# Optimization experiments

Measured on AMD Instinct MI355X. Metric: run time of the kernel, lower is better.

Reference implementation:

```python
import jax, jax.numpy as jnp
import numpy as np

H = 56; W = 56; WS = 7; NW = WS * WS  # 49 tokens per window
HEADS = 8; DIM = 256; HIDDEN = 4 * DIM
SHIFT = NW // 2  # gilbert shift = 24 (shift_size > 0)
SCALE = (DIM // HEADS) ** -0.5
EPS = 1e-5


def _sgn(v):
    return -1 if v < 0 else 1 if v > 0 else 0


def _generate2d(x, y, ax, ay, bx, by, result):
    w = abs(ax + ay); h = abs(bx + by)
    dax, day = _sgn(ax), _sgn(ay); dbx, dby = _sgn(bx), _sgn(by)
    if h == 1 or w == 1:
        if h == 1:
            for _ in range(w):
                result.append((x, y)); x, y = x + dax, y + day
        elif w == 1:
            for _ in range(h):
                result.append((x, y)); x, y = x + dbx, y + dby
        return
    ax2, ay2 = ax // 2, ay // 2; bx2, by2 = bx // 2, by // 2
    w2 = abs(ax2 + ay2); h2 = abs(bx2 + by2)
    if 2 * w > 3 * h:
        if w2 % 2 and w > 2:
            ax2, ay2 = ax2 + dax, ay2 + day
        _generate2d(x, y, ax2, ay2, bx, by, result)
        _generate2d(x + ax2, y + ay2, ax - ax2, ay - ay2, bx, by, result)
    else:
        if h2 % 2 and h > 2:
            bx2, by2 = bx2 + dbx, by2 + dby
        _generate2d(x, y, bx2, by2, ax2, ay2, result)
        _generate2d(x + bx2, y + by2, ax, ay, bx - bx2, by - by2, result)
        _generate2d(x + (ax - dax) + (bx2 - dbx), y + (ay - day) + (by2 - dby),
                    -bx2, -by2, -(ax - ax2), -(ay - ay2), result)


def _gilbert2d(width, height):
    result = []
    if width >= height:
        _generate2d(0, 0, width, 0, 0, height, result)
    else:
        _generate2d(0, 0, 0, height, width, 0, result)
    return result


def _make_rel_index():
    # reverse_map[idx] = (y, x) for gilbert position idx
    path = _gilbert2d(W, H)
    rev = np.zeros((H * W, 2), dtype=np.int64)
    for i, (px, py) in enumerate(path[:H * W]):
        rev[i, 0] = py; rev[i, 1] = px
    pos = np.roll(rev, SHIFT, axis=0)  # shifted block: roll positions by ws^2//2
    n_windows = (H * W) // NW
    pos = pos[:n_windows * NW].reshape(n_windows, NW, 2)
    dh = pos[:, :, 0][:, :, None] - pos[:, :, 0][:, None, :] + (H - 1)
    dw = pos[:, :, 1][:, :, None] - pos[:, :, 1][:, None, :] + (W - 1)
    return (dh * (2 * W - 1) + dw).astype(np.int32)  # (nW, 49, 49)


def setup_inputs() -> dict:
    key = jax.random.key(0)
    ks = jax.random.split(key, 8)
    B, L, C = 32, H * W, DIM
    return {
        "x": jax.random.normal(ks[0], (B, L, C), jnp.float32),
        "qkv_w": jax.random.normal(ks[1], (C, 3 * C), jnp.float32) * 0.02,
        "qkv_b": jnp.zeros((3 * C,), jnp.float32),
        "proj_w": jax.random.normal(ks[2], (C, C), jnp.float32) * 0.02,
        "proj_b": jnp.zeros((C,), jnp.float32),
        "bias_table": jax.random.normal(ks[3], ((2 * H - 1) * (2 * W - 1), HEADS), jnp.float32) * 0.02,
        "norm1_w": jnp.ones((C,), jnp.float32),
        "norm1_b": jnp.zeros((C,), jnp.float32),
        "norm2_w": jnp.ones((C,), jnp.float32),
        "norm2_b": jnp.zeros((C,), jnp.float32),
        "fc1_w": jax.random.normal(ks[4], (C, HIDDEN), jnp.float32) * 0.02,
        "fc1_b": jnp.zeros((HIDDEN,), jnp.float32),
        "fc2_w": jax.random.normal(ks[5], (HIDDEN, C), jnp.float32) * 0.02,
        "fc2_b": jnp.zeros((C,), jnp.float32),
        "rel_index": jnp.asarray(_make_rel_index()),
    }


def _layernorm(x, w, b):
    mu = jnp.mean(x, axis=-1, keepdims=True)
    var = jnp.mean(jnp.square(x - mu), axis=-1, keepdims=True)
    return (x - mu) * jax.lax.rsqrt(var + EPS) * w + b


def reference(x, qkv_w, qkv_b, proj_w, proj_b, bias_table,
              norm1_w, norm1_b, norm2_w, norm2_b,
              fc1_w, fc1_b, fc2_w, fc2_b, rel_index):
    B, L, C = x.shape
    n_win = L // NW
    hd = C // HEADS

    shortcut = x
    h = _layernorm(x, norm1_w, norm1_b)
    # gilbert forward shift along the curve, then window partition
    h = jnp.roll(h, SHIFT, axis=1)
    hw = h.reshape(B * n_win, NW, C)

    qkv = (hw @ qkv_w + qkv_b).reshape(B * n_win, NW, 3, HEADS, hd)
    qkv = jnp.transpose(qkv, (2, 0, 3, 1, 4))  # (3, B*nW, heads, N, hd)
    q, k, v = qkv[0] * SCALE, qkv[1], qkv[2]

    attn = jnp.einsum('bhnd,bhmd->bhnm', q, k)  # (B*nW, heads, 49, 49)
    bias = jnp.transpose(bias_table[rel_index], (0, 3, 1, 2))  # (nW, heads, 49, 49)
    attn = attn.reshape(B, n_win, HEADS, NW, NW) + bias[None]
    attn = jax.nn.softmax(attn, axis=-1).reshape(B * n_win, HEADS, NW, NW)

    out = jnp.einsum('bhnm,bhmd->bhnd', attn, v)
    out = jnp.transpose(out, (0, 2, 1, 3)).reshape(B * n_win, NW, C)
    out = out @ proj_w + proj_b

    # window merge + gilbert reverse shift
    out = out.reshape(B, L, C)
    out = jnp.roll(out, -SHIFT, axis=1)

    x = shortcut + out
    h2 = _layernorm(x, norm2_w, norm2_b)
    h2 = jax.nn.gelu(h2 @ fc1_w + fc1_b, approximate=False) @ fc2_w + fc2_b
    return x + h2
```

## Files before the change

kernel.cpp:

```cpp
#include <hip/hip_runtime.h>
#include <math.h>

typedef unsigned short u16;
typedef __attribute__((ext_vector_type(8))) short bfrag;
typedef __attribute__((ext_vector_type(4))) float f32x4;
typedef __attribute__((ext_vector_type(4))) unsigned short us4;

#define B_SZ 32
#define L_SZ 3136
#define C_SZ 256
#define NHEADS 8
#define HID_SZ 1024
#define NW 49
#define NWIN 64
#define SHIFT 24
#define M_SZ (B_SZ * L_SZ)
#define SCALEF 0.17677669529663687f

__device__ __forceinline__ float bf2f(u16 u) {
  union { unsigned int i; float f; } v; v.i = ((unsigned)u) << 16; return v.f;
}
__device__ __forceinline__ u16 f2bf(float f) {
  union { unsigned int i; float f; } v; v.f = f;
  return (u16)((v.i + 0x7fffu + ((v.i >> 16) & 1u)) >> 16);
}
__device__ __forceinline__ void gload_lds16(const u16* g, u16* l) {
  __builtin_amdgcn_global_load_lds(
      (const __attribute__((address_space(1))) unsigned int*)g,
      (__attribute__((address_space(3))) unsigned int*)l, 16, 0, 0);
}

__global__ void transpose_kernel(const float* __restrict__ in, u16* __restrict__ out,
                                 int K, int N) {
  const int idx = blockIdx.x * 256 + threadIdx.x;
  if (idx >= K * N) return;
  const int n = idx / K;
  const int k = idx - n * K;
  out[idx] = f2bf(in[(size_t)k * N + n]);
}

__global__ void bias_kernel(const float* __restrict__ tab, const int* __restrict__ rel,
                            float* __restrict__ bm) {
  const int idx = blockIdx.x * 256 + threadIdx.x;
  const int tot = NWIN * NHEADS * NW * NW;
  if (idx >= tot) return;
  const int w = idx / (NHEADS * NW * NW);
  const int r = idx - w * (NHEADS * NW * NW);
  const int h = r / (NW * NW);
  const int ij = r - h * (NW * NW);
  bm[idx] = tab[(size_t)rel[w * NW * NW + ij] * NHEADS + h];
}

__global__ __launch_bounds__(256) void ln1_kernel(
    const float* __restrict__ x, const float* __restrict__ w,
    const float* __restrict__ b, u16* __restrict__ out) {
  const int wv = threadIdx.x >> 6;
  const int lane = threadIdx.x & 63;
  const int row0 = blockIdx.x * 16 + wv * 4;
  float4 u[4];
#pragma unroll
  for (int r = 0; r < 4; ++r)
    u[r] = *((const float4*)x + (size_t)(row0 + r) * 64 + lane);
  float s[4], sq[4];
#pragma unroll
  for (int r = 0; r < 4; ++r) {
    s[r]  = u[r].x + u[r].y + u[r].z + u[r].w;
    sq[r] = u[r].x * u[r].x + u[r].y * u[r].y + u[r].z * u[r].z + u[r].w * u[r].w;
  }
#pragma unroll
  for (int d = 1; d < 64; d <<= 1)
#pragma unroll
    for (int r = 0; r < 4; ++r) {
      s[r] += __shfl_xor(s[r], d); sq[r] += __shfl_xor(sq[r], d);
    }
  float wv4[4], bv4[4];
#pragma unroll
  for (int j = 0; j < 4; ++j) { wv4[j] = w[lane * 4 + j]; bv4[j] = b[lane * 4 + j]; }
#pragma unroll
  for (int r = 0; r < 4; ++r) {
    const int row = row0 + r;
    const float mu = s[r] * (1.0f / C_SZ);
    const float rs = rsqrtf(sq[r] * (1.0f / C_SZ) - mu * mu + 1e-5f);
    const int bb = row / L_SZ;
    int l2 = row - bb * L_SZ + SHIFT;
    if (l2 >= L_SZ) l2 -= L_SZ;
    const float vv[4] = {u[r].x, u[r].y, u[r].z, u[r].w};
    us4 ov;
#pragma unroll
    for (int j = 0; j < 4; ++j) ov[j] = f2bf((vv[j] - mu) * rs * wv4[j] + bv4[j]);
    *(us4*)(out + ((size_t)bb * L_SZ + l2) * C_SZ + lane * 4) = ov;
  }
}

__global__ __launch_bounds__(256) void ln2_kernel(
    const u16* __restrict__ x, const float* __restrict__ w,
    const float* __restrict__ b, u16* __restrict__ out) {
  const int wv = threadIdx.x >> 6;
  const int lane = threadIdx.x & 63;
  const int row0 = blockIdx.x * 16 + wv * 4;
  us4 u[4];
#pragma unroll
  for (int r = 0; r < 4; ++r)
    u[r] = *(const us4*)(x + (size_t)(row0 + r) * C_SZ + lane * 4);
  float v[4][4], s[4], sq[4];
#pragma unroll
  for (int r = 0; r < 4; ++r) {
    s[r] = 0.f; sq[r] = 0.f;
#pragma unroll
    for (int j = 0; j < 4; ++j) {
      v[r][j] = bf2f(u[r][j]); s[r] += v[r][j]; sq[r] += v[r][j] * v[r][j];
    }
  }
#pragma unroll
  for (int d = 1; d < 64; d <<= 1)
#pragma unroll
    for (int r = 0; r < 4; ++r) {
      s[r] += __shfl_xor(s[r], d); sq[r] += __shfl_xor(sq[r], d);
    }
  float wv4[4], bv4[4];
#pragma unroll
  for (int j = 0; j < 4; ++j) { wv4[j] = w[lane * 4 + j]; bv4[j] = b[lane * 4 + j]; }
#pragma unroll
  for (int r = 0; r < 4; ++r) {
    const float mu = s[r] * (1.0f / C_SZ);
    const float rs = rsqrtf(sq[r] * (1.0f / C_SZ) - mu * mu + 1e-5f);
    us4 ov;
#pragma unroll
    for (int j = 0; j < 4; ++j) ov[j] = f2bf((v[r][j] - mu) * rs * wv4[j] + bv4[j]);
    *(us4*)(out + (size_t)(row0 + r) * C_SZ + lane * 4) = ov;
  }
}

#define BM 128
#define BN 128
#define BKT 64

template <int MODE>
__global__ __launch_bounds__(256, 2) void gemm_kernel(
    const u16* __restrict__ A, const u16* __restrict__ Bt,
    const float* __restrict__ bias, int N, int K, void* __restrict__ Cout,
    const float* __restrict__ resx, const u16* __restrict__ resb2) {
  __shared__ u16 Als[BM * BKT];
  __shared__ u16 Bls[BN * BKT];
  const int tid = threadIdx.x;
  const int lane = tid & 63;
  const int lr = lane & 15;
  const int lg = lane >> 4;
  const int m0 = blockIdx.y * BM;
  const int n0 = blockIdx.x * BN;
  const int wid = tid >> 6;
  const int wm = (wid >> 1) * 64;
  const int wn = (wid & 1) * 64;

  const int grow = lane >> 3;
  const int gch = (lane & 7) ^ grow;

  const f32x4 fzero = {0.f, 0.f, 0.f, 0.f};
  f32x4 acc[4][4];
#pragma unroll
  for (int i = 0; i < 4; ++i)
#pragma unroll
    for (int j = 0; j < 4; ++j) acc[i][j] = fzero;

  const u16* Agl = A + (size_t)m0 * K + gch * 8;
  const u16* Bgl = Bt + (size_t)n0 * K + gch * 8;

  for (int k0 = 0; k0 < K; k0 += BKT) {
#pragma unroll
    for (int g = 0; g < 4; ++g) {
      const int rbase = wid * 32 + g * 8;
      gload_lds16(Agl + (size_t)(rbase + grow) * K + k0, Als + rbase * 64);
      gload_lds16(Bgl + (size_t)(rbase + grow) * K + k0, Bls + rbase * 64);
    }
    __syncthreads();
#pragma unroll
    for (int s = 0; s < 2; ++s) {
      const int kg = s * 4 + lg;
      bfrag af[4], bfv[4];
#pragma unroll
      for (int m = 0; m < 4; ++m) {
        const int r = wm + m * 16 + lr;
        af[m] = *(const bfrag*)(Als + r * 64 + ((kg ^ (r & 7)) * 8));
      }
#pragma unroll
      for (int n = 0; n < 4; ++n) {
        const int r = wn + n * 16 + lr;
        bfv[n] = *(const bfrag*)(Bls + r * 64 + ((kg ^ (r & 7)) * 8));
      }
#pragma unroll
      for (int m = 0; m < 4; ++m)
#pragma unroll
        for (int n = 0; n < 4; ++n)
          acc[m][n] = __builtin_amdgcn_mfma_f32_16x16x32_bf16(af[m], bfv[n],
                                                              acc[m][n], 0, 0, 0);
    }
    __syncthreads();
  }

  float bv4[4];
#pragma unroll
  for (int n = 0; n < 4; ++n) bv4[n] = bias[n0 + wn + n * 16 + lr];

#pragma unroll
  for (int m = 0; m < 4; ++m) {
#pragma unroll
    for (int i = 0; i < 4; ++i) {
      const int row = m0 + wm + m * 16 + lg * 4 + i;
      if (MODE == 1) {
        const int bb = row / L_SZ;
        int l2 = row - bb * L_SZ - SHIFT;
        if (l2 < 0) l2 += L_SZ;
        const size_t orow = (size_t)bb * L_SZ + l2;
#pragma unroll
        for (int n = 0; n < 4; ++n) {
          const int col = n0 + wn + n * 16 + lr;
          ((u16*)Cout)[orow * N + col] =
              f2bf(resx[orow * N + col] + acc[m][n][i] + bv4[n]);
        }
      } else {
#pragma unroll
        for (int n = 0; n < 4; ++n) {
          const int col = n0 + wn + n * 16 + lr;
          float v = acc[m][n][i] + bv4[n];
          if (MODE == 2) v = 0.5f * v * (1.0f + erff(v * 0.70710678f));
          if (MODE == 3) {
            v += bf2f(resb2[(size_t)row * N + col]);
            ((float*)Cout)[(size_t)row * N + col] = v;
          } else {
            ((u16*)Cout)[(size_t)row * N + col] = f2bf(v);
          }
        }
      }
    }
  }
}

__global__ __launch_bounds__(256) void attn_kernel(const u16* __restrict__ qkv,
                                                   const float* __restrict__ bm,
                                                   u16* __restrict__ out, int widx0) {
  __shared__ u16 Pls[4][64 * 72];
  const int wl = blockIdx.x;
  const int w = (widx0 + wl) & (NWIN - 1);
  const int wv = threadIdx.x >> 6;
  const int lane = threadIdx.x & 63;
  const int lr = lane & 15;
  const int lg = lane >> 4;
  const size_t base = (size_t)wl * NW;
  u16* P = Pls[wv];
  const f32x4 fzero = {0.f, 0.f, 0.f, 0.f};

  for (int rep = 0; rep < 2; ++rep) {
    const int h = wv * 2 + rep;
    bfrag qf[4], kf[4];
#pragma unroll
    for (int m = 0; m < 4; ++m) {
      int r = m * 16 + lr; if (r > NW - 1) r = NW - 1;
      qf[m] = *(const bfrag*)(qkv + (base + r) * 768 + h * 32 + lg * 8);
      kf[m] = *(const bfrag*)(qkv + (base + r) * 768 + 256 + h * 32 + lg * 8);
    }
    f32x4 s[4][4];
#pragma unroll
    for (int m = 0; m < 4; ++m)
#pragma unroll
      for (int n = 0; n < 4; ++n)
        s[m][n] = __builtin_amdgcn_mfma_f32_16x16x32_bf16(qf[m], kf[n], fzero, 0, 0, 0);

    const float* bh = bm + (size_t)(w * NHEADS + h) * (NW * NW);
#pragma unroll
    for (int m = 0; m < 4; ++m) {
#pragma unroll
      for (int i = 0; i < 4; ++i) {
        const int row = m * 16 + lg * 4 + i;
        const int brow = row > NW - 1 ? NW - 1 : row;
        float vals[4];
#pragma unroll
        for (int n = 0; n < 4; ++n) {
          const int c = n * 16 + lr;
          vals[n] = (c < NW) ? (s[m][n][i] * SCALEF + bh[brow * NW + c]) : -1e30f;
        }
        float mx = fmaxf(fmaxf(vals[0], vals[1]), fmaxf(vals[2], vals[3]));
#pragma unroll
        for (int d = 1; d < 16; d <<= 1) mx = fmaxf(mx, __shfl_xor(mx, d));
        float sum = 0.f;
#pragma unroll
        for (int n = 0; n < 4; ++n) { vals[n] = __expf(vals[n] - mx); sum += vals[n]; }
#pragma unroll
        for (int d = 1; d < 16; d <<= 1) sum += __shfl_xor(sum, d);
        const float inv = 1.0f / sum;
#pragma unroll
        for (int n = 0; n < 4; ++n)
          P[row * 72 + n * 16 + lr] = f2bf(vals[n] * inv);
      }
    }
    f32x4 o[4][2];
#pragma unroll
    for (int m = 0; m < 4; ++m) { o[m][0] = fzero; o[m][1] = fzero; }
#pragma unroll
    for (int s2 = 0; s2 < 2; ++s2) {
      bfrag pf[4];
#pragma unroll
      for (int m = 0; m < 4; ++m)
        pf[m] = *(const bfrag*)(P + (m * 16 + lr) * 72 + s2 * 32 + lg * 8);
#pragma unroll
      for (int n = 0; n < 2; ++n) {
        bfrag vf;
#pragma unroll
        for (int i = 0; i < 8; ++i) {
          int kk = s2 * 32 + lg * 8 + i; if (kk > NW - 1) kk = NW - 1;
          vf[i] = *(const short*)(qkv + (base + kk) * 768 + 512 + h * 32 + n * 16 + lr);
        }
#pragma unroll
        for (int m = 0; m < 4; ++m)
          o[m][n] = __builtin_amdgcn_mfma_f32_16x16x32_bf16(pf[m], vf, o[m][n], 0, 0, 0);
      }
    }
#pragma unroll
    for (int m = 0; m < 4; ++m)
#pragma unroll
      for (int i = 0; i < 4; ++i) {
        const int row = m * 16 + lg * 4 + i;
        if (row < NW) {
#pragma unroll
          for (int n = 0; n < 2; ++n)
            out[(base + row) * C_SZ + h * 32 + n * 16 + lr] = f2bf(o[m][n][i]);
        }
      }
  }
}

extern "C" void kernel_launch(void* const* d_in, const int* in_sizes, int n_in,
                              void* d_out, int out_size, void* d_ws, size_t ws_size,
                              hipStream_t stream) {
  (void)in_sizes; (void)n_in; (void)out_size;
  const float* x     = (const float*)d_in[0];
  const float* qkvw  = (const float*)d_in[1];
  const float* qkvb  = (const float*)d_in[2];
  const float* projw = (const float*)d_in[3];
  const float* projb = (const float*)d_in[4];
  const float* btab  = (const float*)d_in[5];
  const float* n1w   = (const float*)d_in[6];
  const float* n1b   = (const float*)d_in[7];
  const float* n2w   = (const float*)d_in[8];
  const float* n2b   = (const float*)d_in[9];
  const float* fc1w  = (const float*)d_in[10];
  const float* fc1b  = (const float*)d_in[11];
  const float* fc2w  = (const float*)d_in[12];
  const float* fc2b  = (const float*)d_in[13];
  const int* rel     = (const int*)d_in[14];

  char* ws = (char*)d_ws;
  size_t off = 0;
  auto alloc = [&](size_t bytes) -> char* {
    char* p = ws + off; off += (bytes + 255) & ~(size_t)255; return p;
  };
  u16* qkvwT   = (u16*)alloc((size_t)768 * 256 * 2);
  u16* projwT  = (u16*)alloc((size_t)256 * 256 * 2);
  u16* fc1wT   = (u16*)alloc((size_t)1024 * 256 * 2);
  u16* fc2wT   = (u16*)alloc((size_t)256 * 1024 * 2);
  float* biasm = (float*)alloc((size_t)NWIN * NHEADS * NW * NW * 4);
  u16* bufh    = (u16*)alloc((size_t)M_SZ * C_SZ * 2);
  u16* x2b     = (u16*)alloc((size_t)M_SZ * C_SZ * 2);

  const size_t full_scr = (size_t)M_SZ * HID_SZ * 2;
  const int nch = (ws_size >= off + full_scr + 256) ? 1 : 4;
  const int mch = M_SZ / nch;
  const int wch = (B_SZ * NWIN) / nch;
  u16* scratch2 = (u16*)alloc((size_t)mch * HID_SZ * 2);

  transpose_kernel<<<(256 * 768 + 255) / 256, 256, 0, stream>>>(qkvw, qkvwT, 256, 768);
  transpose_kernel<<<(256 * 256 + 255) / 256, 256, 0, stream>>>(projw, projwT, 256, 256);
  transpose_kernel<<<(256 * 1024 + 255) / 256, 256, 0, stream>>>(fc1w, fc1wT, 256, 1024);
  transpose_kernel<<<(1024 * 256 + 255) / 256, 256, 0, stream>>>(fc2w, fc2wT, 1024, 256);
  bias_kernel<<<(NWIN * NHEADS * NW * NW + 255) / 256, 256, 0, stream>>>(btab, rel, biasm);

  ln1_kernel<<<M_SZ / 16, 256, 0, stream>>>(x, n1w, n1b, bufh);

  for (int c = 0; c < nch; ++c) {
    const size_t roff = (size_t)c * mch;
    gemm_kernel<0><<<dim3(768 / BN, mch / BM), 256, 0, stream>>>(
        bufh + roff * C_SZ, qkvwT, qkvb, 768, 256, scratch2, nullptr, nullptr);
    attn_kernel<<<wch, 256, 0, stream>>>(scratch2, biasm, bufh + roff * C_SZ, c * wch);
  }

  gemm_kernel<1><<<dim3(256 / BN, M_SZ / BM), 256, 0, stream>>>(
      bufh, projwT, projb, 256, 256, x2b, x, nullptr);

  for (int q = 0; q < nch; ++q) {
    const size_t roff = (size_t)q * mch;
    ln2_kernel<<<mch / 16, 256, 0, stream>>>(x2b + roff * C_SZ, n2w, n2b,
                                             bufh + roff * C_SZ);
    gemm_kernel<2><<<dim3(1024 / BN, mch / BM), 256, 0, stream>>>(
        bufh + roff * C_SZ, fc1wT, fc1b, 1024, 256, scratch2, nullptr, nullptr);
    gemm_kernel<3><<<dim3(256 / BN, mch / BM), 256, 0, stream>>>(
        scratch2, fc2wT, fc2b, 256, 1024, (float*)d_out + roff * C_SZ,
        nullptr, x2b + roff * C_SZ);
  }
}
```

Measured before the change: 511.1 us.

## Fuse LayerNorm1, QKV projection and window attention into one per-window kernel

Replaces the separate ln1, QKV GEMM and attention kernels with a single kernel per (batch, window) block. The block layer-norms its 49 shifted rows into swizzled LDS, and each wave computes its heads' Q/K/V tiles with MFMA straight into LDS, with V stored transposed. It then runs softmax attention from LDS. This removes the global round-trips for the normalized activations and the large QKV intermediate. In exchange, QKV weights are re-read from global/L2 by every block, 64-row tiles pad the 49 tokens, and LDS use (~80KB) limits occupancy.

```diff
diff --git a/kernel.cpp b/kernel.cpp
--- a/kernel.cpp
+++ b/kernel.cpp
@@ -51,44 +51,175 @@
   bm[idx] = tab[(size_t)rel[w * NW * NW + ij] * NHEADS + h];
 }
 
-__global__ __launch_bounds__(256) void ln1_kernel(
-    const float* __restrict__ x, const float* __restrict__ w,
-    const float* __restrict__ b, u16* __restrict__ out) {
+__global__ __launch_bounds__(256, 2) void qkvattn_kernel(
+    const float* __restrict__ x, const float* __restrict__ n1w,
+    const float* __restrict__ n1b, const u16* __restrict__ qkvwT,
+    const float* __restrict__ qkvb, const float* __restrict__ bm,
+    u16* __restrict__ out) {
+  __shared__ u16 hs[64 * 256];
+  __shared__ u16 wscr[4][3 * 64 * 32];
+  const int widx = blockIdx.x;
+  const int b = widx >> 6;
+  const int w = widx & 63;
   const int wv = threadIdx.x >> 6;
   const int lane = threadIdx.x & 63;
-  const int row0 = blockIdx.x * 16 + wv * 4;
-  float4 u[4];
-#pragma unroll
-  for (int r = 0; r < 4; ++r)
-    u[r] = *((const float4*)x + (size_t)(row0 + r) * 64 + lane);
-  float s[4], sq[4];
-#pragma unroll
-  for (int r = 0; r < 4; ++r) {
-    s[r]  = u[r].x + u[r].y + u[r].z + u[r].w;
-    sq[r] = u[r].x * u[r].x + u[r].y * u[r].y + u[r].z * u[r].z + u[r].w * u[r].w;
-  }
-#pragma unroll
-  for (int d = 1; d < 64; d <<= 1)
-#pragma unroll
-    for (int r = 0; r < 4; ++r) {
-      s[r] += __shfl_xor(s[r], d); sq[r] += __shfl_xor(sq[r], d);
-    }
+  const int lr = lane & 15;
+  const int lg = lane >> 4;
+  const f32x4 fzero = {0.f, 0.f, 0.f, 0.f};
+
   float wv4[4], bv4[4];
 #pragma unroll
-  for (int j = 0; j < 4; ++j) { wv4[j] = w[lane * 4 + j]; bv4[j] = b[lane * 4 + j]; }
-#pragma unroll
-  for (int r = 0; r < 4; ++r) {
-    const int row = row0 + r;
-    const float mu = s[r] * (1.0f / C_SZ);
-    const float rs = rsqrtf(sq[r] * (1.0f / C_SZ) - mu * mu + 1e-5f);
-    const int bb = row / L_SZ;
-    int l2 = row - bb * L_SZ + SHIFT;
-    if (l2 >= L_SZ) l2 -= L_SZ;
-    const float vv[4] = {u[r].x, u[r].y, u[r].z, u[r].w};
-    us4 ov;
-#pragma unroll
-    for (int j = 0; j < 4; ++j) ov[j] = f2bf((vv[j] - mu) * rs * wv4[j] + bv4[j]);
-    *(us4*)(out + ((size_t)bb * L_SZ + l2) * C_SZ + lane * 4) = ov;
+  for (int j = 0; j < 4; ++j) { wv4[j] = n1w[lane * 4 + j]; bv4[j] = n1b[lane * 4 + j]; }
+  for (int r = wv; r < 64; r += 4) {
+    u16* hp = hs + r * 256 + (((lane >> 1) ^ (r & 7)) << 3) + ((lane & 1) << 2);
+    if (r < NW) {
+      int l = w * NW + r - SHIFT;
+      if (l < 0) l += L_SZ;
+      const float4 u = *((const float4*)x + ((size_t)b * L_SZ + l) * 64 + lane);
+      float s = u.x + u.y + u.z + u.w;
+      float sq = u.x * u.x + u.y * u.y + u.z * u.z + u.w * u.w;
+#pragma unroll
+      for (int d = 1; d < 64; d <<= 1) { s += __shfl_xor(s, d); sq += __shfl_xor(sq, d); }
+      const float mu = s * (1.0f / C_SZ);
+      const float rs = rsqrtf(sq * (1.0f / C_SZ) - mu * mu + 1e-5f);
+      const float vv[4] = {u.x, u.y, u.z, u.w};
+      us4 ov;
+#pragma unroll
+      for (int j = 0; j < 4; ++j) ov[j] = f2bf((vv[j] - mu) * rs * wv4[j] + bv4[j]);
+      *(us4*)hp = ov;
+    } else {
+      us4 z = {0, 0, 0, 0};
+      *(us4*)hp = z;
+    }
+  }
+  __syncthreads();
+
+  u16* q   = wscr[wv];
+  u16* kk_ = q + 64 * 32;
+  u16* vT  = q + 2 * 64 * 32;
+  u16* P   = q;
+
+  for (int rep = 0; rep < 2; ++rep) {
+    const int hh = wv * 2 + rep;
+#pragma unroll
+    for (int mat = 0; mat < 3; ++mat) {
+      f32x4 a4[4][2];
+#pragma unroll
+      for (int m = 0; m < 4; ++m) { a4[m][0] = fzero; a4[m][1] = fzero; }
+      const u16* wbase = qkvwT + (size_t)(mat * 256 + hh * 32) * 256;
+#pragma unroll
+      for (int kt = 0; kt < 8; ++kt) {
+        bfrag bf[2], af[4];
+#pragma unroll
+        for (int n = 0; n < 2; ++n)
+          bf[n] = *(const bfrag*)(wbase + (size_t)(n * 16 + lr) * 256 + kt * 32 + lg * 8);
+#pragma unroll
+        for (int m = 0; m < 4; ++m) {
+          const int r = m * 16 + lr;
+          af[m] = *(const bfrag*)(hs + r * 256 + (((kt * 4 + lg) ^ (r & 7)) << 3));
+        }
+#pragma unroll
+        for (int m = 0; m < 4; ++m)
+#pragma unroll
+          for (int n = 0; n < 2; ++n)
+            a4[m][n] = __builtin_amdgcn_mfma_f32_16x16x32_bf16(af[m], bf[n],
+                                                               a4[m][n], 0, 0, 0);
+      }
+      float bb[2];
+#pragma unroll
+      for (int n = 0; n < 2; ++n) bb[n] = qkvb[mat * 256 + hh * 32 + n * 16 + lr];
+      u16* dst = (mat == 0) ? q : (mat == 1) ? kk_ : vT;
+#pragma unroll
+      for (int m = 0; m < 4; ++m)
+#pragma unroll
+        for (int n = 0; n < 2; ++n)
+#pragma unroll
+          for (int i = 0; i < 4; ++i) {
+            const int r2 = m * 16 + lg * 4 + i;
+            const int c = n * 16 + lr;
+            const u16 val = f2bf(a4[m][n][i] + bb[n]);
+            if (mat < 2) dst[r2 * 32 + (((c >> 3) ^ (r2 & 3)) << 3) + (c & 7)] = val;
+            else         dst[c * 64 + (((r2 >> 3) ^ (c & 7)) << 3) + (r2 & 7)] = val;
+          }
+    }
+    bfrag qf[4], kf[4];
+#pragma unroll
+    for (int m = 0; m < 4; ++m) {
+      const int r = m * 16 + lr;
+      qf[m] = *(const bfrag*)(q + r * 32 + ((lg ^ (r & 3)) << 3));
+      kf[m] = *(const bfrag*)(kk_ + r * 32 + ((lg ^ (r & 3)) << 3));
+    }
+    f32x4 S[4][4];
+#pragma unroll
+    for (int m = 0; m < 4; ++m)
+#pragma unroll
+      for (int n = 0; n < 4; ++n)
+        S[m][n] = __builtin_amdgcn_mfma_f32_16x16x32_bf16(qf[m], kf[n], fzero, 0, 0, 0);
+
+    const float* bh = bm + (size_t)(w * NHEADS + hh) * (NW * NW);
+#pragma unroll
+    for (int m = 0; m < 4; ++m) {
+#pragma unroll
+      for (int i = 0; i < 4; ++i) {
+        const int row = m * 16 + lg * 4 + i;
+        const int brow = row > NW - 1 ? NW - 1 : row;
+        float vals[4];
+#pragma unroll
+        for (int n = 0; n < 4; ++n) {
+          const int c = n * 16 + lr;
+          vals[n] = (c < NW) ? (S[m][n][i] * SCALEF + bh[brow * NW + c]) : -1e30f;
+        }
+        float mx = fmaxf(fmaxf(vals[0], vals[1]), fmaxf(vals[2], vals[3]));
+#pragma unroll
+        for (int d = 1; d < 16; d <<= 1) mx = fmaxf(mx, __shfl_xor(mx, d));
+        float sum = 0.f;
+#pragma unroll
+        for (int n = 0; n < 4; ++n) { vals[n] = __expf(vals[n] - mx); sum += vals[n]; }
+#pragma unroll
+        for (int d = 1; d < 16; d <<= 1) sum += __shfl_xor(sum, d);
+        const float inv = 1.0f / sum;
+#pragma unroll
+        for (int n = 0; n < 4; ++n) {
+          const int c = n * 16 + lr;
+          P[row * 64 + (((c >> 3) ^ (row & 7)) << 3) + (c & 7)] = f2bf(vals[n] * inv);
+        }
+      }
+    }
+    f32x4 o[4][2];
+#pragma unroll
+    for (int m = 0; m < 4; ++m) { o[m][0] = fzero; o[m][1] = fzero; }
+#pragma unroll
+    for (int s2 = 0; s2 < 2; ++s2) {
+      bfrag pf[4], vf[2];
+#pragma unroll
+      for (int m = 0; m < 4; ++m) {
+        const int r = m * 16 + lr;
+        pf[m] = *(const bfrag*)(P + r * 64 + (((s2 * 4 + lg) ^ (r & 7)) << 3));
+      }
+#pragma unroll
+      for (int n = 0; n < 2; ++n) {
+        const int dc = n * 16 + lr;
+        vf[n] = *(const bfrag*)(vT + dc * 64 + (((s2 * 4 + lg) ^ (dc & 7)) << 3));
+      }
+#pragma unroll
+      for (int m = 0; m < 4; ++m)
+#pragma unroll
+        for (int n = 0; n < 2; ++n)
+          o[m][n] = __builtin_amdgcn_mfma_f32_16x16x32_bf16(pf[m], vf[n],
+                                                            o[m][n], 0, 0, 0);
+    }
+#pragma unroll
+    for (int m = 0; m < 4; ++m)
+#pragma unroll
+      for (int i = 0; i < 4; ++i) {
+        const int row = m * 16 + lg * 4 + i;
+        if (row < NW) {
+#pragma unroll
+          for (int n = 0; n < 2; ++n)
+            out[((size_t)widx * NW + row) * C_SZ + hh * 32 + n * 16 + lr] =
+                f2bf(o[m][n][i]);
+        }
+      }
   }
 }
 
@@ -232,99 +363,6 @@
         }
       }
     }
-  }
-}
-
-__global__ __launch_bounds__(256) void attn_kernel(const u16* __restrict__ qkv,
-                                                   const float* __restrict__ bm,
-                                                   u16* __restrict__ out, int widx0) {
-  __shared__ u16 Pls[4][64 * 72];
-  const int wl = blockIdx.x;
-  const int w = (widx0 + wl) & (NWIN - 1);
-  const int wv = threadIdx.x >> 6;
-  const int lane = threadIdx.x & 63;
-  const int lr = lane & 15;
-  const int lg = lane >> 4;
-  const size_t base = (size_t)wl * NW;
-  u16* P = Pls[wv];
-  const f32x4 fzero = {0.f, 0.f, 0.f, 0.f};
-
-  for (int rep = 0; rep < 2; ++rep) {
-    const int h = wv * 2 + rep;
-    bfrag qf[4], kf[4];
-#pragma unroll
-    for (int m = 0; m < 4; ++m) {
-      int r = m * 16 + lr; if (r > NW - 1) r = NW - 1;
-      qf[m] = *(const bfrag*)(qkv + (base + r) * 768 + h * 32 + lg * 8);
-      kf[m] = *(const bfrag*)(qkv + (base + r) * 768 + 256 + h * 32 + lg * 8);
-    }
-    f32x4 s[4][4];
-#pragma unroll
-    for (int m = 0; m < 4; ++m)
-#pragma unroll
-      for (int n = 0; n < 4; ++n)
-        s[m][n] = __builtin_amdgcn_mfma_f32_16x16x32_bf16(qf[m], kf[n], fzero, 0, 0, 0);
-
-    const float* bh = bm + (size_t)(w * NHEADS + h) * (NW * NW);
-#pragma unroll
-    for (int m = 0; m < 4; ++m) {
-#pragma unroll
-      for (int i = 0; i < 4; ++i) {
-        const int row = m * 16 + lg * 4 + i;
-        const int brow = row > NW - 1 ? NW - 1 : row;
-        float vals[4];
-#pragma unroll
-        for (int n = 0; n < 4; ++n) {
-          const int c = n * 16 + lr;
-          vals[n] = (c < NW) ? (s[m][n][i] * SCALEF + bh[brow * NW + c]) : -1e30f;
-        }
-        float mx = fmaxf(fmaxf(vals[0], vals[1]), fmaxf(vals[2], vals[3]));
-#pragma unroll
-        for (int d = 1; d < 16; d <<= 1) mx = fmaxf(mx, __shfl_xor(mx, d));
-        float sum = 0.f;
-#pragma unroll
-        for (int n = 0; n < 4; ++n) { vals[n] = __expf(vals[n] - mx); sum += vals[n]; }
-#pragma unroll
-        for (int d = 1; d < 16; d <<= 1) sum += __shfl_xor(sum, d);
-        const float inv = 1.0f / sum;
-#pragma unroll
-        for (int n = 0; n < 4; ++n)
-          P[row * 72 + n * 16 + lr] = f2bf(vals[n] * inv);
-      }
-    }
-    f32x4 o[4][2];
-#pragma unroll
-    for (int m = 0; m < 4; ++m) { o[m][0] = fzero; o[m][1] = fzero; }
-#pragma unroll
-    for (int s2 = 0; s2 < 2; ++s2) {
-      bfrag pf[4];
-#pragma unroll
-      for (int m = 0; m < 4; ++m)
-        pf[m] = *(const bfrag*)(P + (m * 16 + lr) * 72 + s2 * 32 + lg * 8);
-#pragma unroll
-      for (int n = 0; n < 2; ++n) {
-        bfrag vf;
-#pragma unroll
-        for (int i = 0; i < 8; ++i) {
-          int kk = s2 * 32 + lg * 8 + i; if (kk > NW - 1) kk = NW - 1;
-          vf[i] = *(const short*)(qkv + (base + kk) * 768 + 512 + h * 32 + n * 16 + lr);
-        }
-#pragma unroll
-        for (int m = 0; m < 4; ++m)
-          o[m][n] = __builtin_amdgcn_mfma_f32_16x16x32_bf16(pf[m], vf, o[m][n], 0, 0, 0);
-      }
-    }
-#pragma unroll
-    for (int m = 0; m < 4; ++m)
-#pragma unroll
-      for (int i = 0; i < 4; ++i) {
-        const int row = m * 16 + lg * 4 + i;
-        if (row < NW) {
-#pragma unroll
-          for (int n = 0; n < 2; ++n)
-            out[(base + row) * C_SZ + h * 32 + n * 16 + lr] = f2bf(o[m][n][i]);
-        }
-      }
   }
 }
 
@@ -364,7 +402,6 @@
   const size_t full_scr = (size_t)M_SZ * HID_SZ * 2;
   const int nch = (ws_size >= off + full_scr + 256) ? 1 : 4;
   const int mch = M_SZ / nch;
-  const int wch = (B_SZ * NWIN) / nch;
   u16* scratch2 = (u16*)alloc((size_t)mch * HID_SZ * 2);
 
   transpose_kernel<<<(256 * 768 + 255) / 256, 256, 0, stream>>>(qkvw, qkvwT, 256, 768);
@@ -373,14 +410,8 @@
   transpose_kernel<<<(1024 * 256 + 255) / 256, 256, 0, stream>>>(fc2w, fc2wT, 1024, 256);
   bias_kernel<<<(NWIN * NHEADS * NW * NW + 255) / 256, 256, 0, stream>>>(btab, rel, biasm);
 
-  ln1_kernel<<<M_SZ / 16, 256, 0, stream>>>(x, n1w, n1b, bufh);
-
-  for (int c = 0; c < nch; ++c) {
-    const size_t roff = (size_t)c * mch;
-    gemm_kernel<0><<<dim3(768 / BN, mch / BM), 256, 0, stream>>>(
-        bufh + roff * C_SZ, qkvwT, qkvb, 768, 256, scratch2, nullptr, nullptr);
-    attn_kernel<<<wch, 256, 0, stream>>>(scratch2, biasm, bufh + roff * C_SZ, c * wch);
-  }
+  qkvattn_kernel<<<B_SZ * NWIN, 256, 0, stream>>>(x, n1w, n1b, qkvwT, qkvb,
+                                                  biasm, bufh);
 
   gemm_kernel<1><<<dim3(256 / BN, M_SZ / BM), 256, 0, stream>>>(
       bufh, projwT, projb, 256, 256, x2b, x, nullptr);
```

After: 537.5 us. +5.2%, slower.

## Write V transposed from QKV GEMM epilogue and split attention per head-half

Applied to the files above, without the earlier changes.

The QKV GEMM epilogue now writes Q and K into a 512-wide buffer and scatters V into a per-window, per-head transposed layout [d][64 tokens]. The attention kernel can then load V fragments as contiguous 8-element vectors instead of eight scalar strided loads. Attention is launched once over all windows, with two blocks per window each handling four heads, instead of one block looping over two heads per wave. The chunking of QKV and attention is removed, which assumes the workspace holds the full QK and V buffers. The transposed V scatter writes are uncoalesced, and V padding tokens 49..63 are never written, leaving uninitialized values that are multiplied by zero probabilities.

```diff
diff --git a/kernel.cpp b/kernel.cpp
--- a/kernel.cpp
+++ b/kernel.cpp
@@ -139,7 +139,8 @@
 __global__ __launch_bounds__(256, 2) void gemm_kernel(
     const u16* __restrict__ A, const u16* __restrict__ Bt,
     const float* __restrict__ bias, int N, int K, void* __restrict__ Cout,
-    const float* __restrict__ resx, const u16* __restrict__ resb2) {
+    const float* __restrict__ resx, u16* __restrict__ vt,
+    const u16* __restrict__ resb2) {
   __shared__ u16 Als[BM * BKT];
   __shared__ u16 Bls[BN * BKT];
   const int tid = threadIdx.x;
@@ -217,17 +218,38 @@
           ((u16*)Cout)[orow * N + col] =
               f2bf(resx[orow * N + col] + acc[m][n][i] + bv4[n]);
         }
-      } else {
+      } else if (MODE == 2) {
 #pragma unroll
         for (int n = 0; n < 4; ++n) {
           const int col = n0 + wn + n * 16 + lr;
           float v = acc[m][n][i] + bv4[n];
-          if (MODE == 2) v = 0.5f * v * (1.0f + erff(v * 0.70710678f));
-          if (MODE == 3) {
-            v += bf2f(resb2[(size_t)row * N + col]);
-            ((float*)Cout)[(size_t)row * N + col] = v;
-          } else {
-            ((u16*)Cout)[(size_t)row * N + col] = f2bf(v);
+          v = 0.5f * v * (1.0f + erff(v * 0.70710678f));
+          ((u16*)Cout)[(size_t)row * N + col] = f2bf(v);
+        }
+      } else if (MODE == 3) {
+#pragma unroll
+        for (int n = 0; n < 4; ++n) {
+          const int col = n0 + wn + n * 16 + lr;
+          ((float*)Cout)[(size_t)row * N + col] =
+              acc[m][n][i] + bv4[n] + bf2f(resb2[(size_t)row * N + col]);
+        }
+      } else {
+        if (n0 + wn < 512) {
+#pragma unroll
+          for (int n = 0; n < 4; ++n) {
+            const int col = n0 + wn + n * 16 + lr;
+            ((u16*)Cout)[(size_t)row * 512 + col] = f2bf(acc[m][n][i] + bv4[n]);
+          }
+        } else {
+          const unsigned widx = (unsigned)row / 49u;
+          const int kk = row - (int)widx * 49;
+#pragma unroll
+          for (int n = 0; n < 4; ++n) {
+            const int col = n0 + wn + n * 16 + lr - 512;
+            const int hh = col >> 5;
+            const int d = col & 31;
+            vt[(((size_t)widx * NHEADS + hh) * 32 + d) * 64 + kk] =
+                f2bf(acc[m][n][i] + bv4[n]);
           }
         }
       }
@@ -235,97 +257,95 @@
   }
 }
 
-__global__ __launch_bounds__(256) void attn_kernel(const u16* __restrict__ qkv,
+__global__ __launch_bounds__(256) void attn_kernel(const u16* __restrict__ qk,
+                                                   const u16* __restrict__ vt,
                                                    const float* __restrict__ bm,
-                                                   u16* __restrict__ out, int widx0) {
+                                                   u16* __restrict__ out) {
   __shared__ u16 Pls[4][64 * 72];
-  const int wl = blockIdx.x;
-  const int w = (widx0 + wl) & (NWIN - 1);
+  const int widx = blockIdx.x >> 1;
+  const int half = blockIdx.x & 1;
+  const int w = widx & (NWIN - 1);
   const int wv = threadIdx.x >> 6;
   const int lane = threadIdx.x & 63;
   const int lr = lane & 15;
   const int lg = lane >> 4;
-  const size_t base = (size_t)wl * NW;
+  const size_t base = (size_t)widx * NW;
   u16* P = Pls[wv];
   const f32x4 fzero = {0.f, 0.f, 0.f, 0.f};
-
-  for (int rep = 0; rep < 2; ++rep) {
-    const int h = wv * 2 + rep;
-    bfrag qf[4], kf[4];
-#pragma unroll
-    for (int m = 0; m < 4; ++m) {
-      int r = m * 16 + lr; if (r > NW - 1) r = NW - 1;
-      qf[m] = *(const bfrag*)(qkv + (base + r) * 768 + h * 32 + lg * 8);
-      kf[m] = *(const bfrag*)(qkv + (base + r) * 768 + 256 + h * 32 + lg * 8);
-    }
-    f32x4 s[4][4];
+  const int h = half * 4 + wv;
+
+  bfrag qf[4], kf[4];
+#pragma unroll
+  for (int m = 0; m < 4; ++m) {
+    int r = m * 16 + lr; if (r > NW - 1) r = NW - 1;
+    qf[m] = *(const bfrag*)(qk + (base + r) * 512 + h * 32 + lg * 8);
+    kf[m] = *(const bfrag*)(qk + (base + r) * 512 + 256 + h * 32 + lg * 8);
+  }
+  f32x4 s[4][4];
+#pragma unroll
+  for (int m = 0; m < 4; ++m)
+#pragma unroll
+    for (int n = 0; n < 4; ++n)
+      s[m][n] = __builtin_amdgcn_mfma_f32_16x16x32_bf16(qf[m], kf[n], fzero, 0, 0, 0);
+
+  const float* bh = bm + (size_t)(w * NHEADS + h) * (NW * NW);
+#pragma unroll
+  for (int m = 0; m < 4; ++m) {
+#pragma unroll
+    for (int i = 0; i < 4; ++i) {
+      const int row = m * 16 + lg * 4 + i;
+      const int brow = row > NW - 1 ? NW - 1 : row;
+      float vals[4];
+#pragma unroll
+      for (int n = 0; n < 4; ++n) {
+        const int c = n * 16 + lr;
+        vals[n] = (c < NW) ? (s[m][n][i] * SCALEF + bh[brow * NW + c]) : -1e30f;
+      }
+      float mx = fmaxf(fmaxf(vals[0], vals[1]), fmaxf(vals[2], vals[3]));
+#pragma unroll
+      for (int d = 1; d < 16; d <<= 1) mx = fmaxf(mx, __shfl_xor(mx, d));
+      float sum = 0.f;
+#pragma unroll
+      for (int n = 0; n < 4; ++n) { vals[n] = __expf(vals[n] - mx); sum += vals[n]; }
+#pragma unroll
+      for (int d = 1; d < 16; d <<= 1) sum += __shfl_xor(sum, d);
+      const float inv = 1.0f / sum;
+#pragma unroll
+      for (int n = 0; n < 4; ++n)
+        P[row * 72 + n * 16 + lr] = f2bf(vals[n] * inv);
+    }
+  }
+  const u16* vth = vt + ((size_t)widx * NHEADS + h) * 32 * 64;
+  f32x4 o[4][2];
+#pragma unroll
+  for (int m = 0; m < 4; ++m) { o[m][0] = fzero; o[m][1] = fzero; }
+#pragma unroll
+  for (int s2 = 0; s2 < 2; ++s2) {
+    bfrag pf[4], vf[2];
 #pragma unroll
     for (int m = 0; m < 4; ++m)
-#pragma unroll
-      for (int n = 0; n < 4; ++n)
-        s[m][n] = __builtin_amdgcn_mfma_f32_16x16x32_bf16(qf[m], kf[n], fzero, 0, 0, 0);
-
-    const float* bh = bm + (size_t)(w * NHEADS + h) * (NW * NW);
-#pragma unroll
-    for (int m = 0; m < 4; ++m) {
-#pragma unroll
-      for (int i = 0; i < 4; ++i) {
-        const int row = m * 16 + lg * 4 + i;
-        const int brow = row > NW - 1 ? NW - 1 : row;
-        float vals[4];
-#pragma unroll
-        for (int n = 0; n < 4; ++n) {
-          const int c = n * 16 + lr;
-          vals[n] = (c < NW) ? (s[m][n][i] * SCALEF + bh[brow * NW + c]) : -1e30f;
-        }
-        float mx = fmaxf(fmaxf(vals[0], vals[1]), fmaxf(vals[2], vals[3]));
-#pragma unroll
-        for (int d = 1; d < 16; d <<= 1) mx = fmaxf(mx, __shfl_xor(mx, d));
-        float sum = 0.f;
-#pragma unroll
-        for (int n = 0; n < 4; ++n) { vals[n] = __expf(vals[n] - mx); sum += vals[n]; }
-#pragma unroll
-        for (int d = 1; d < 16; d <<= 1) sum += __shfl_xor(sum, d);
-        const float inv = 1.0f / sum;
-#pragma unroll
-        for (int n = 0; n < 4; ++n)
-          P[row * 72 + n * 16 + lr] = f2bf(vals[n] * inv);
+      pf[m] = *(const bfrag*)(P + (m * 16 + lr) * 72 + s2 * 32 + lg * 8);
+#pragma unroll
+    for (int n = 0; n < 2; ++n)
+      vf[n] = *(const bfrag*)(vth + (size_t)(n * 16 + lr) * 64 + s2 * 32 + lg * 8);
+#pragma unroll
+    for (int m = 0; m < 4; ++m)
+#pragma unroll
+      for (int n = 0; n < 2; ++n)
+        o[m][n] = __builtin_amdgcn_mfma_f32_16x16x32_bf16(pf[m], vf[n],
+                                                          o[m][n], 0, 0, 0);
+  }
+#pragma unroll
+  for (int m = 0; m < 4; ++m)
+#pragma unroll
+    for (int i = 0; i < 4; ++i) {
+      const int row = m * 16 + lg * 4 + i;
+      if (row < NW) {
+#pragma unroll
+        for (int n = 0; n < 2; ++n)
+          out[(base + row) * C_SZ + h * 32 + n * 16 + lr] = f2bf(o[m][n][i]);
       }
     }
-    f32x4 o[4][2];
-#pragma unroll
-    for (int m = 0; m < 4; ++m) { o[m][0] = fzero; o[m][1] = fzero; }
-#pragma unroll
-    for (int s2 = 0; s2 < 2; ++s2) {
-      bfrag pf[4];
-#pragma unroll
-      for (int m = 0; m < 4; ++m)
-        pf[m] = *(const bfrag*)(P + (m * 16 + lr) * 72 + s2 * 32 + lg * 8);
-#pragma unroll
-      for (int n = 0; n < 2; ++n) {
-        bfrag vf;
-#pragma unroll
-        for (int i = 0; i < 8; ++i) {
-          int kk = s2 * 32 + lg * 8 + i; if (kk > NW - 1) kk = NW - 1;
-          vf[i] = *(const short*)(qkv + (base + kk) * 768 + 512 + h * 32 + n * 16 + lr);
-        }
-#pragma unroll
-        for (int m = 0; m < 4; ++m)
-          o[m][n] = __builtin_amdgcn_mfma_f32_16x16x32_bf16(pf[m], vf, o[m][n], 0, 0, 0);
-      }
-    }
-#pragma unroll
-    for (int m = 0; m < 4; ++m)
-#pragma unroll
-      for (int i = 0; i < 4; ++i) {
-        const int row = m * 16 + lg * 4 + i;
-        if (row < NW) {
-#pragma unroll
-          for (int n = 0; n < 2; ++n)
-            out[(base + row) * C_SZ + h * 32 + n * 16 + lr] = f2bf(o[m][n][i]);
-        }
-      }
-  }
 }
 
 extern "C" void kernel_launch(void* const* d_in, const int* in_sizes, int n_in,
@@ -361,11 +381,16 @@
   u16* bufh    = (u16*)alloc((size_t)M_SZ * C_SZ * 2);
   u16* x2b     = (u16*)alloc((size_t)M_SZ * C_SZ * 2);
 
+  char* tail = ws + off;
+  u16* qkbuf = (u16*)tail;
+  const size_t qk_bytes = (size_t)M_SZ * 512 * 2;
+  u16* vtbuf = (u16*)(tail + qk_bytes);
+  const size_t tail_attn = qk_bytes + (size_t)B_SZ * NWIN * NHEADS * 32 * 64 * 2;
+  u16* scratch2 = (u16*)tail;
   const size_t full_scr = (size_t)M_SZ * HID_SZ * 2;
-  const int nch = (ws_size >= off + full_scr + 256) ? 1 : 4;
+  const size_t tail_need1 = full_scr > tail_attn ? full_scr : tail_attn;
+  const int nch = (ws_size >= off + tail_need1) ? 1 : 4;
   const int mch = M_SZ / nch;
-  const int wch = (B_SZ * NWIN) / nch;
-  u16* scratch2 = (u16*)alloc((size_t)mch * HID_SZ * 2);
 
   transpose_kernel<<<(256 * 768 + 255) / 256, 256, 0, stream>>>(qkvw, qkvwT, 256, 768);
   transpose_kernel<<<(256 * 256 + 255) / 256, 256, 0, stream>>>(projw, projwT, 256, 256);
@@ -375,24 +400,22 @@
 
   ln1_kernel<<<M_SZ / 16, 256, 0, stream>>>(x, n1w, n1b, bufh);
 
-  for (int c = 0; c < nch; ++c) {
-    const size_t roff = (size_t)c * mch;
-    gemm_kernel<0><<<dim3(768 / BN, mch / BM), 256, 0, stream>>>(
-        bufh + roff * C_SZ, qkvwT, qkvb, 768, 256, scratch2, nullptr, nullptr);
-    attn_kernel<<<wch, 256, 0, stream>>>(scratch2, biasm, bufh + roff * C_SZ, c * wch);
-  }
+  gemm_kernel<0><<<dim3(768 / BN, M_SZ / BM), 256, 0, stream>>>(
+      bufh, qkvwT, qkvb, 768, 256, qkbuf, nullptr, vtbuf, nullptr);
+
+  attn_kernel<<<B_SZ * NWIN * 2, 256, 0, stream>>>(qkbuf, vtbuf, biasm, bufh);
 
   gemm_kernel<1><<<dim3(256 / BN, M_SZ / BM), 256, 0, stream>>>(
-      bufh, projwT, projb, 256, 256, x2b, x, nullptr);
+      bufh, projwT, projb, 256, 256, x2b, x, nullptr, nullptr);
 
   for (int q = 0; q < nch; ++q) {
     const size_t roff = (size_t)q * mch;
     ln2_kernel<<<mch / 16, 256, 0, stream>>>(x2b + roff * C_SZ, n2w, n2b,
                                              bufh + roff * C_SZ);
-    gemm_kernel<2><<<dim3(1024 / BN, mch / BM), 256, 0, stream>>>(
-        bufh + roff * C_SZ, fc1wT, fc1b, 1024, 256, scratch2, nullptr, nullptr);
+    gemm_kernel<2><<<dim3(HID_SZ / BN, mch / BM), 256, 0, stream>>>(
+        bufh + roff * C_SZ, fc1wT, fc1b, 1024, 256, scratch2, nullptr, nullptr, nullptr);
     gemm_kernel<3><<<dim3(256 / BN, mch / BM), 256, 0, stream>>>(
         scratch2, fc2wT, fc2b, 256, 1024, (float*)d_out + roff * C_SZ,
-        nullptr, x2b + roff * C_SZ);
-  }
-}
+        nullptr, nullptr, x2b + roff * C_SZ);
+  }
+}
```

Result: no change. 513.1 us (+0.4%).
